# Kernel optimization log

Hardware: AMD Instinct MI355X
Metric: run time of the kernel (lower is better)

## Reference

```python
import jax, jax.numpy as jnp
import numpy as np

DIM = 1024
NUM_HEAD = 16
DIM_HEAD = DIM // NUM_HEAD
MAX_SEQ_LEN = 4096
RMS_EPS = 1.1920928955078125e-07  # torch nn.RMSNorm default eps = finfo(fp32).eps
LIN_EPS = 1e-6
PAD_VAL = 1.0
THETA = 10000.0


def rmsnorm(x, g):
    return x * jax.lax.rsqrt(jnp.mean(x * x, axis=-1, keepdims=True) + RMS_EPS) * g


def setup_inputs() -> dict:
    key = jax.random.key(0)
    ks = jax.random.split(key, 20)
    B, L, C, D = 4, 2048, 256, DIM
    s = 1.0 / np.sqrt(D)
    inp = {
        "x": jax.random.normal(ks[0], (B, L, D), jnp.float32),
        "context": jax.random.normal(ks[1], (B, C, D), jnp.float32),
        "attn_mask": jax.random.randint(ks[2], (B, L, L), 0, 2).astype(bool),
        "start_pos": jax.random.randint(ks[3], (B,), 0, MAX_SEQ_LEN - L).astype(jnp.int64),
        "Wqkv": jax.random.normal(ks[4], (D, 3 * D), jnp.float32) * s,
        "bqkv": jax.random.normal(ks[5], (3 * D,), jnp.float32) * 0.01,
        "g_q": jnp.ones((D,), jnp.float32),
        "g_k": jnp.ones((D,), jnp.float32),
        "cWqkv": jax.random.normal(ks[6], (D, 3 * D), jnp.float32) * s,
        "cbqkv": jax.random.normal(ks[7], (3 * D,), jnp.float32) * 0.01,
        "cg_q": jnp.ones((D,), jnp.float32),
        "cg_k": jnp.ones((D,), jnp.float32),
        "Wout": jax.random.normal(ks[8], (D, D), jnp.float32) * s,
        "bout": jax.random.normal(ks[9], (D,), jnp.float32) * 0.01,
        "g_out": jnp.ones((D,), jnp.float32),
        "cWout": jax.random.normal(ks[10], (D, D), jnp.float32) * s,
        "cbout": jax.random.normal(ks[11], (D,), jnp.float32) * 0.01,
        "cg_out": jnp.ones((D,), jnp.float32),
    }
    return inp


def _freqs(pos_indices):
    # pos_indices: (B, L) int
    inv = 1.0 / (THETA ** (jnp.arange(0, DIM_HEAD, 2, dtype=jnp.float32) / DIM_HEAD))  # (DH/2,)
    ang = pos_indices.astype(jnp.float32)[..., None] * inv  # (B, L, DH/2)
    return jnp.cos(ang), jnp.sin(ang)


def _apply_rope(t, cos, sin):
    # t: (B, H, L, DH); cos/sin: (B, L, DH/2) -> broadcast over head
    B, H, L, DH = t.shape
    tr = t.reshape(B, H, L, DH // 2, 2)
    t0, t1 = tr[..., 0], tr[..., 1]
    c = cos[:, None]  # (B,1,L,DH/2)
    s = sin[:, None]
    out = jnp.stack([t0 * c - t1 * s, t0 * s + t1 * c], axis=-1)
    return out.reshape(B, H, L, DH)


def _split_heads(t):
    B, L, D = t.shape
    return t.reshape(B, L, NUM_HEAD, DIM_HEAD).transpose(0, 2, 1, 3)


def _augment_mask(m, C):
    # m: (B, L, L) bool -> (B, L+C, L+C) bool
    B, L, _ = m.shape
    c_to_seq = jnp.broadcast_to(jnp.any(m, axis=1, keepdims=True), (B, C, L))
    seq_to_c = jnp.broadcast_to(jnp.any(m, axis=2, keepdims=True), (B, L, C))
    c_to_c = jnp.ones((B, C, C), bool)
    top = jnp.concatenate([m, seq_to_c], axis=2)
    bot = jnp.concatenate([c_to_seq, c_to_c], axis=2)
    return jnp.concatenate([top, bot], axis=1)


def reference(x, context, attn_mask, start_pos, Wqkv, bqkv, g_q, g_k,
              cWqkv, cbqkv, cg_q, cg_k, Wout, bout, g_out, cWout, cbout, cg_out):
    B, L, D = x.shape
    C = context.shape[1]

    q, k, v = jnp.split(x @ Wqkv + bqkv, 3, axis=-1)
    q = rmsnorm(q, g_q)
    k = rmsnorm(k, g_k)
    q, k, v = _split_heads(q), _split_heads(k), _split_heads(v)  # (B,H,L,DH)

    pos = start_pos[:, None] + jnp.arange(L, dtype=start_pos.dtype)[None]  # (B,L)
    cos, sin = _freqs(pos)
    q = _apply_rope(q, cos, sin)
    k = _apply_rope(k, cos, sin)

    cq, ck, cv = jnp.split(context @ cWqkv + cbqkv, 3, axis=-1)
    cq = rmsnorm(cq, cg_q)
    ck = rmsnorm(ck, cg_k)
    cq, ck, cv = _split_heads(cq), _split_heads(ck), _split_heads(cv)

    q = jnp.concatenate([q, cq], axis=2)  # (B,H,S,DH), S=L+C
    k = jnp.concatenate([k, ck], axis=2)
    v = jnp.concatenate([v, cv], axis=2)

    full_mask = _augment_mask(attn_mask, C)[:, None]  # (B,1,S,S)

    # linear attention: ReLU feature map + padded-value trick
    qf = jax.nn.relu(q)
    kf = jax.nn.relu(k)
    k_mask = full_mask[:, :, 0, :][..., None].astype(kf.dtype)  # (B,1,S,1)
    kf = kf * k_mask
    vpad = jnp.pad(v, ((0, 0), (0, 0), (0, 0), (0, 1)), constant_values=PAD_VAL)  # (B,H,S,DH+1)
    vk = jnp.einsum('bhse,bhsd->bhed', vpad, kf)        # (B,H,DH+1,DH)
    res = jnp.einsum('bhed,bhqd->bhqe', vk, qf)          # (B,H,S,DH+1)
    attn = res[..., :-1] / (res[..., -1:] + LIN_EPS)     # (B,H,S,DH)

    attn = attn.transpose(0, 2, 1, 3).reshape(B, L + C, D)
    x_out = rmsnorm(attn[:, :L] @ Wout + bout, g_out)
    c_out = rmsnorm(attn[:, L:] @ cWout + cbout, cg_out)
    return x_out, c_out
```

## Files before the change

### kernel.cpp

```cpp
#include <hip/hip_runtime.h>

typedef __bf16 bf16;
typedef __bf16 bf16x4 __attribute__((ext_vector_type(4)));
typedef __bf16 bf16x8 __attribute__((ext_vector_type(8)));
typedef float  floatx4 __attribute__((ext_vector_type(4)));

#define L_SEQ   2048
#define C_SEQ   256
#define S_SEQ   2304
#define NBATCH  4
#define NHEAD   16
#define DHEAD   64
#define DMODEL  1024
#define RMS_EPS 1.1920928955078125e-07f
#define LIN_EPS 1e-6f

__device__ __forceinline__ void gload_lds16(const void* g, void* l) {
  __builtin_amdgcn_global_load_lds(
      (const __attribute__((address_space(1))) void*)g,
      (__attribute__((address_space(3))) void*)l, 16, 0, 0);
}

__device__ __forceinline__ void transpose_job64(
    const float* __restrict__ src, bf16* __restrict__ dst,
    int R, int C, int tb, bf16 (*tile)[65]) {
  int tilesx = C >> 6;
  int c0 = (tb % tilesx) * 64, r0 = (tb / tilesx) * 64;
  int tx = threadIdx.x & 15, ty = threadIdx.x >> 4;
#pragma unroll
  for (int it = 0; it < 4; it++) {
    int rl = ty + it * 16;
    floatx4 v = *(const floatx4*)(src + (size_t)(r0 + rl) * C + c0 + tx * 4);
#pragma unroll
    for (int j = 0; j < 4; j++) tile[tx * 4 + j][rl] = (bf16)v[j];
  }
  __syncthreads();
#pragma unroll
  for (int it = 0; it < 4; it++) {
    int i = ty + it * 16;
    bf16x4 o = *(const bf16x4*)&tile[i][tx * 4];
    *(bf16x4*)(dst + (size_t)(c0 + i) * R + r0 + tx * 4) = o;
  }
}

__device__ __forceinline__ void convert_job(
    const float* __restrict__ src, bf16* __restrict__ dst, int tb) {
  size_t i = ((size_t)tb * 256 + threadIdx.x) * 8;
  floatx4 a = *(const floatx4*)(src + i);
  floatx4 b = *(const floatx4*)(src + i + 4);
  bf16x8 o;
#pragma unroll
  for (int j = 0; j < 4; j++) { o[j] = (bf16)a[j]; o[4 + j] = (bf16)b[j]; }
  *(bf16x8*)(dst + i) = o;
}

__global__ __launch_bounds__(256) void prep(
    const float* __restrict__ Wqkv, const float* __restrict__ cWqkv,
    const float* __restrict__ x, const float* __restrict__ ctx,
    const int* __restrict__ mask, const int* __restrict__ spos,
    bf16* __restrict__ WqkvT, bf16* __restrict__ cWqkvT,
    bf16* __restrict__ xbf, bf16* __restrict__ cbf,
    float* __restrict__ rope, int* __restrict__ anym) {
  __shared__ bf16 tile[64][65];
  __shared__ int sh;
  int b = blockIdx.x;
  if (b < 768) { transpose_job64(Wqkv, WqkvT, 1024, 3072, b, tile); return; }
  b -= 768;
  if (b < 768) { transpose_job64(cWqkv, cWqkvT, 1024, 3072, b, tile); return; }
  b -= 768;
  if (b < 4096) { convert_job(x, xbf, b); return; }
  b -= 4096;
  if (b < 512) { convert_job(ctx, cbf, b); return; }
  b -= 512;
  if (b < 2048) {
    int t = threadIdx.x;
    int tok = b * 4 + (t >> 6);
    int bb = tok >> 11, s = tok & 2047;
    int j = t & 63, fi = j >> 1;
    float ang = (float)(spos[bb] + s) * expf((float)fi * -0.28782313662425572f);
    rope[(size_t)tok * 64 + j] = (j & 1) ? sinf(ang) : cosf(ang);
    return;
  }
  b -= 2048;
  int a = 0;
  size_t base = (size_t)b * L_SEQ * L_SEQ;
  for (int j = threadIdx.x; j < L_SEQ; j += 256) a |= mask[base + j];
  if (threadIdx.x == 0) sh = 0;
  __syncthreads();
  if (a) atomicOr(&sh, 1);
  __syncthreads();
  if (threadIdx.x == 0) anym[b] = sh;
}

__global__ __launch_bounds__(512, 2) void gemm_qkv8(
    const bf16* __restrict__ A1, const bf16* __restrict__ A2,
    const bf16* __restrict__ B1t, const bf16* __restrict__ B2t,
    const float* __restrict__ bias1, const float* __restrict__ bias2,
    bf16* __restrict__ qs, bf16* __restrict__ ks, bf16* __restrict__ vs,
    int K, int ybound, int rpb1, int soff1, int rpb2, int soff2) {
  __shared__ bf16 As[2][256 * 64];
  __shared__ bf16 Bs[2][256 * 64];

  int nwg = gridDim.x * gridDim.y;
  int wg = blockIdx.y * gridDim.x + blockIdx.x;
  int cpx = nwg >> 3;
  wg = (wg & 7) * cpx + (wg >> 3);
  int bx = wg % gridDim.x, by = wg / gridDim.x;
  int n0 = bx * 256;
  const bf16 *Ap, *Bt;
  const float* bias;
  int m0, rpb, soff;
  if (by < ybound) {
    Ap = A1; Bt = B1t; bias = bias1; m0 = by * 256; rpb = rpb1; soff = soff1;
  } else {
    Ap = A2; Bt = B2t; bias = bias2; m0 = (by - ybound) * 256; rpb = rpb2; soff = soff2;
  }

  int t = threadIdx.x, lane = t & 63, w = t >> 6;
  int wr = w >> 2, wc = w & 3;
  int l16 = lane & 15, l4 = lane >> 4;

  int lr = lane >> 3;
  int lcol = ((lane & 7) ^ lr) << 3;
  const bf16* Ag = Ap + (size_t)(m0 + lr) * K + lcol;
  const bf16* Bg = Bt + (size_t)(n0 + lr) * K + lcol;

  int cB0 = w * 2;
  int cB1 = 16 + w * 2;
  int cAX = ((w & 4) << 2) + (w & 3) * 2;
  int cAY = 8 + cAX;

  auto stg = [&](const bf16* G, bf16* Ldst, int c0, int kb) {
#pragma unroll
    for (int j = 0; j < 2; j++) {
      int c = c0 + j;
      gload_lds16(G + (size_t)(c * 8) * K + kb, (char*)Ldst + c * 1024);
    }
  };
  auto ldf = [&](const bf16* S, int row, int ks) {
    return *(const bf16x8*)&S[row * 64 + ((((ks << 2) + l4) ^ (l16 & 7)) << 3)];
  };

  floatx4 acc[8][4] = {};
  int NT = K >> 6;
  stg(Bg, Bs[0], cB0, 0);  stg(Bg, Bs[0], cB1, 0);
  stg(Ag, As[0], cAX, 0);  stg(Ag, As[0], cAY, 0);
  if (NT > 1) {
    stg(Bg, Bs[1], cB0, 64); stg(Bg, Bs[1], cB1, 64);
    stg(Ag, As[1], cAX, 64);
  }
  asm volatile("s_waitcnt vmcnt(6)" ::: "memory");
  __builtin_amdgcn_s_barrier();

  int pb = 0;
  bf16x8 bfr[4][2];
  for (int tt = 0; tt < NT; ++tt) {
    int kb = tt << 6;
    const bf16* Asp = As[pb];
    const bf16* Bsp = Bs[pb];
#pragma unroll
    for (int p = 0; p < 4; ++p) {
      if (p == 0) {
#pragma unroll
        for (int nt = 0; nt < 4; nt++) {
          bfr[nt][0] = ldf(Bsp, wc * 64 + nt * 16 + l16, 0);
          bfr[nt][1] = ldf(Bsp, wc * 64 + nt * 16 + l16, 1);
        }
      }
      int ar = wr * 128 + p * 32 + l16;
      bf16x8 a00 = ldf(Asp, ar, 0);
      bf16x8 a01 = ldf(Asp, ar, 1);
      bf16x8 a10 = ldf(Asp, ar + 16, 0);
      bf16x8 a11 = ldf(Asp, ar + 16, 1);
      if (p == 0)      { if (tt + 1 < NT) stg(Ag, As[pb ^ 1], cAY, kb + 64); }
      else if (p == 1) { if (tt + 2 < NT) stg(Bg, Bs[pb], cB0, kb + 128); }
      else if (p == 2) { if (tt + 2 < NT) stg(Bg, Bs[pb], cB1, kb + 128); }
      else             { if (tt + 2 < NT) stg(Ag, As[pb], cAX, kb + 128); }
      __builtin_amdgcn_s_barrier();
      __builtin_amdgcn_s_setprio(1);
      int mt = p * 2;
#pragma unroll
      for (int nt = 0; nt < 4; nt++) {
        acc[mt][nt]     = __builtin_amdgcn_mfma_f32_16x16x32_bf16(a00, bfr[nt][0], acc[mt][nt], 0, 0, 0);
        acc[mt][nt]     = __builtin_amdgcn_mfma_f32_16x16x32_bf16(a01, bfr[nt][1], acc[mt][nt], 0, 0, 0);
        acc[mt + 1][nt] = __builtin_amdgcn_mfma_f32_16x16x32_bf16(a10, bfr[nt][0], acc[mt + 1][nt], 0, 0, 0);
        acc[mt + 1][nt] = __builtin_amdgcn_mfma_f32_16x16x32_bf16(a11, bfr[nt][1], acc[mt + 1][nt], 0, 0, 0);
      }
      __builtin_amdgcn_s_setprio(0);
      if (p == 3) {
        if (tt + 2 < NT) asm volatile("s_waitcnt vmcnt(6)" ::: "memory");
        else             asm volatile("s_waitcnt vmcnt(0)" ::: "memory");
      }
      __builtin_amdgcn_s_barrier();
    }
    pb ^= 1;
  }

#pragma unroll
  for (int mt = 0; mt < 8; mt++)
#pragma unroll
    for (int nt = 0; nt < 4; nt++) {
      int col = n0 + wc * 64 + nt * 16 + l16;
      float bval = bias[col];
      int which = col >> 10;
      int h = (col >> 6) & 15;
      int dh = col & 63;
      int rmask = (1 << rpb) - 1;
      if (which == 2) {
        int rw0 = m0 + wr * 128 + mt * 16 + l4 * 4;
        int b = rw0 >> rpb;
        int s = soff + (rw0 & rmask);
        bf16x4 o;
#pragma unroll
        for (int r = 0; r < 4; r++) o[r] = (bf16)(acc[mt][nt][r] + bval);
        *(bf16x4*)(vs + ((size_t)(b * NHEAD + h) * DHEAD + dh) * S_SEQ + s) = o;
      } else {
        bf16* dst = which == 0 ? qs : ks;
#pragma unroll
        for (int r = 0; r < 4; r++) {
          int rw = m0 + wr * 128 + mt * 16 + l4 * 4 + r;
          int b = rw >> rpb;
          int s = soff + (rw & rmask);
          dst[((size_t)(b * NHEAD + h) * S_SEQ + s) * DHEAD + dh] =
              (bf16)(acc[mt][nt][r] + bval);
        }
      }
    }
}

template <bool SCATTER>
__global__ __launch_bounds__(256) void gemm_bias(
    const bf16* __restrict__ A1, const bf16* __restrict__ A2,
    const bf16* __restrict__ B1t, const bf16* __restrict__ B2t,
    const float* __restrict__ bias1, const float* __restrict__ bias2,
    bf16* __restrict__ C1, bf16* __restrict__ C2,
    bf16* __restrict__ qs, bf16* __restrict__ ks, bf16* __restrict__ vs,
    int N, int K, int ybound,
    int rpb1, int soff1, int rpb2, int soff2) {
  __shared__ bf16 As[2][4096];
  __shared__ bf16 Bs[2][4096];
  int nwg = gridDim.x * gridDim.y;
  int wg = blockIdx.y * gridDim.x + blockIdx.x;
  int cpx = nwg >> 3;
  wg = (wg & 7) * cpx + (wg >> 3);
  int bx = wg % gridDim.x, by = wg / gridDim.x;
  int n0 = bx * 128;
  const bf16 *Ap, *Bt;
  const float* bias;
  bf16* Cp;
  int m0, rpb, soff;
  if (by < ybound) {
    Ap = A1; Bt = B1t; bias = bias1; Cp = C1;
    m0 = by * 128; rpb = rpb1; soff = soff1;
  } else {
    Ap = A2; Bt = B2t; bias = bias2; Cp = C2;
    m0 = (by - ybound) * 128; rpb = rpb2; soff = soff2;
  }
  int t = threadIdx.x, lane = t & 63, w = t >> 6;
  int wm = (w & 1) * 64, wn = (w >> 1) * 64;
  int l16 = lane & 15, l4 = lane >> 4;
  int crow = w * 32 + (lane >> 2);
  int scol = ((((lane & 3) - ((lane >> 3) & 3)) & 3)) << 3;
  const bf16* Ab = Ap + (size_t)(m0 + crow) * K + scol;
  const bf16* Bb = Bt + (size_t)(n0 + crow) * K + scol;
  auto stage = [&](int buf, int kb) {
#pragma unroll
    for (int j = 0; j < 2; j++) {
      gload_lds16(Ab + (size_t)(j * 16) * K + kb, (char*)As[buf] + (w * 2 + j) * 1024);
      gload_lds16(Bb + (size_t)(j * 16) * K + kb, (char*)Bs[buf] + (w * 2 + j) * 1024);
    }
  };
  int co = ((l4 + ((l16 >> 1) & 3)) & 3) << 3;
  int rba = (wm + l16) * 32 + co;
  int rbb = (wn + l16) * 32 + co;
  floatx4 acc[4][4] = {};
  stage(0, 0);
  __syncthreads();
  int NTt = K >> 5;
  for (int tt = 0; tt < NTt; ++tt) {
    int p = tt & 1;
    if (tt + 1 < NTt) stage(p ^ 1, (tt + 1) << 5);
    bf16x8 bfr[4];
#pragma unroll
    for (int nt = 0; nt < 4; nt++) bfr[nt] = *(const bf16x8*)&Bs[p][rbb + nt * 512];
    __builtin_amdgcn_s_setprio(1);
#pragma unroll
    for (int mt = 0; mt < 4; mt++) {
      bf16x8 a = *(const bf16x8*)&As[p][rba + mt * 512];
#pragma unroll
      for (int nt = 0; nt < 4; nt++)
        acc[mt][nt] = __builtin_amdgcn_mfma_f32_16x16x32_bf16(a, bfr[nt], acc[mt][nt], 0, 0, 0);
    }
    __builtin_amdgcn_s_setprio(0);
    __syncthreads();
  }
#pragma unroll
  for (int mt = 0; mt < 4; mt++)
#pragma unroll
    for (int nt = 0; nt < 4; nt++) {
      int col = n0 + wn + nt * 16 + l16;
      float bval = bias[col];
      if constexpr (SCATTER) {
        int which = col >> 10;
        int h = (col >> 6) & 15;
        int dh = col & 63;
        int rmask = (1 << rpb) - 1;
        if (which == 2) {
          int rw0 = m0 + wm + mt * 16 + l4 * 4;
          int b = rw0 >> rpb;
          int s = soff + (rw0 & rmask);
          bf16x4 o;
#pragma unroll
          for (int r = 0; r < 4; r++) o[r] = (bf16)(acc[mt][nt][r] + bval);
          *(bf16x4*)(vs + ((size_t)(b * NHEAD + h) * DHEAD + dh) * S_SEQ + s) = o;
        } else {
          bf16* dst = which == 0 ? qs : ks;
#pragma unroll
          for (int r = 0; r < 4; r++) {
            int rw = m0 + wm + mt * 16 + l4 * 4 + r;
            int b = rw >> rpb;
            int s = soff + (rw & rmask);
            dst[((size_t)(b * NHEAD + h) * S_SEQ + s) * DHEAD + dh] =
                (bf16)(acc[mt][nt][r] + bval);
          }
        }
      } else {
#pragma unroll
        for (int r = 0; r < 4; r++) {
          int rw = m0 + wm + mt * 16 + l4 * 4 + r;
          Cp[(size_t)rw * N + col] = (bf16)(acc[mt][nt][r] + bval);
        }
      }
    }
}

__global__ __launch_bounds__(256) void qkv_post(
    bf16* __restrict__ qs, bf16* __restrict__ ks,
    const int* __restrict__ mask, const float* __restrict__ rope,
    const int* __restrict__ anym,
    const float* __restrict__ g_q, const float* __restrict__ g_k,
    const float* __restrict__ cg_q, const float* __restrict__ cg_k,
    const float* __restrict__ Wout, const float* __restrict__ cWout,
    bf16* __restrict__ WoutT, bf16* __restrict__ cWoutT,
    float* __restrict__ vkw) {
  __shared__ bf16 tile[64][65];
  __shared__ float red[8];
  int blk = blockIdx.x, t = threadIdx.x;
  if (blk >= 4608) {
    int b = blk - 4608;
    if (b < 256) { transpose_job64(Wout, WoutT, 1024, 1024, b, tile); return; }
    b -= 256;
    if (b < 256) { transpose_job64(cWout, cWoutT, 1024, 1024, b, tile); return; }
    b -= 256;
    int i = b * 1024 + t * 4;
    *(floatx4*)(vkw + i) = floatx4{0.f, 0.f, 0.f, 0.f};
    return;
  }
  int tt = t & 127, tsel = t >> 7;
  int g = blk * 2 + tsel;
  bool is_ctx = g >= NBATCH * L_SEQ;
  int b, s;
  const float *gq, *gk;
  float mval;
  if (!is_ctx) {
    b = g >> 11;
    int l = g & 2047;
    s = l;
    mval = mask[(size_t)b * L_SEQ * L_SEQ + l] ? 1.f : 0.f;
    gq = g_q; gk = g_k;
  } else {
    int gg = g - NBATCH * L_SEQ;
    b = gg >> 8;
    s = L_SEQ + (gg & 255);
    mval = anym[b] ? 1.f : 0.f;
    gq = cg_q; gk = cg_k;
  }
  int d0 = tt * 8;
  int h = tt >> 3, dh = (tt & 7) * 8;
  size_t base = ((size_t)(b * NHEAD + h) * S_SEQ + s) * DHEAD + dh;
  bf16x8 q8 = *(const bf16x8*)(qs + base);
  bf16x8 k8 = *(const bf16x8*)(ks + base);
  float qv[8], kv[8], pq = 0.f, pk = 0.f;
#pragma unroll
  for (int i = 0; i < 8; i++) {
    qv[i] = (float)q8[i]; kv[i] = (float)k8[i];
    pq += qv[i] * qv[i];  pk += kv[i] * kv[i];
  }
  int w = t >> 6;
  for (int off = 32; off > 0; off >>= 1) {
    pq += __shfl_down(pq, off, 64);
    pk += __shfl_down(pk, off, 64);
  }
  if ((t & 63) == 0) { red[w] = pq; red[4 + w] = pk; }
  __syncthreads();
  float sq = red[tsel * 2] + red[tsel * 2 + 1];
  float sk = red[4 + tsel * 2] + red[4 + tsel * 2 + 1];
  float scq = rsqrtf(sq * (1.f / DMODEL) + RMS_EPS);
  float sck = rsqrtf(sk * (1.f / DMODEL) + RMS_EPS);
#pragma unroll
  for (int i = 0; i < 8; i++) {
    qv[i] *= scq * gq[d0 + i];
    kv[i] *= sck * gk[d0 + i];
  }
  if (!is_ctx) {
    floatx4 ta = *(const floatx4*)&rope[((size_t)g) * 64 + dh];
    floatx4 tb = *(const floatx4*)&rope[((size_t)g) * 64 + dh + 4];
#pragma unroll
    for (int pr = 0; pr < 4; pr++) {
      float cc = pr < 2 ? ta[2 * pr] : tb[2 * (pr - 2)];
      float ss = pr < 2 ? ta[2 * pr + 1] : tb[2 * (pr - 2) + 1];
      float t0 = qv[2 * pr], t1 = qv[2 * pr + 1];
      qv[2 * pr]     = t0 * cc - t1 * ss;
      qv[2 * pr + 1] = t0 * ss + t1 * cc;
      t0 = kv[2 * pr]; t1 = kv[2 * pr + 1];
      kv[2 * pr]     = t0 * cc - t1 * ss;
      kv[2 * pr + 1] = t0 * ss + t1 * cc;
    }
  }
  bf16x8 qo, ko;
#pragma unroll
  for (int i = 0; i < 8; i++) {
    qo[i] = (bf16)fmaxf(qv[i], 0.f);
    ko[i] = (bf16)(fmaxf(kv[i], 0.f) * mval);
  }
  *(bf16x8*)(qs + base) = qo;
  *(bf16x8*)(ks + base) = ko;
}

#define VK_CH   12
#define VK_SPAN (S_SEQ / VK_CH)
__global__ __launch_bounds__(256) void vk_mfma(
    const bf16* __restrict__ vT, const bf16* __restrict__ kf,
    float* __restrict__ vk) {
  __shared__ bf16 Vs[2][64][40];
  __shared__ bf16 Ks[2][64][40];
  int bh = blockIdx.x / VK_CH, chunk = blockIdx.x % VK_CH;
  int t = threadIdx.x, lane = t & 63, w = t >> 6;
  int l16 = lane & 15, l4 = lane >> 4;
  const bf16* vp = vT + (size_t)bh * DHEAD * S_SEQ;
  const bf16* kp = kf + (size_t)bh * S_SEQ * DHEAD;
  int s_begin = chunk * VK_SPAN;
  int ve = t >> 2, vso = (t & 3) * 8;
  int ks_s = t & 31, kd0 = (t >> 5) * 8;
  floatx4 acc[4] = {};
  float dsum[8] = {};
  bf16x8 vv = *(const bf16x8*)(vp + (size_t)ve * S_SEQ + s_begin + vso);
  bf16x8 kv = *(const bf16x8*)(kp + (size_t)(s_begin + ks_s) * DHEAD + kd0);
  for (int st = 0; st < VK_SPAN; st += 32) {
    int cur = (st >> 5) & 1;
    *(bf16x8*)&Vs[cur][ve][vso] = vv;
#pragma unroll
    for (int j = 0; j < 8; j++) {
      Ks[cur][kd0 + j][ks_s] = kv[j];
      dsum[j] += (float)kv[j];
    }
    if (st + 32 < VK_SPAN) {
      int s0 = s_begin + st + 32;
      vv = *(const bf16x8*)(vp + (size_t)ve * S_SEQ + s0 + vso);
      kv = *(const bf16x8*)(kp + (size_t)(s0 + ks_s) * DHEAD + kd0);
    }
    __syncthreads();
    bf16x8 af = *(const bf16x8*)&Vs[cur][w * 16 + l16][l4 * 8];
#pragma unroll
    for (int nt = 0; nt < 4; nt++) {
      bf16x8 bfr = *(const bf16x8*)&Ks[cur][nt * 16 + l16][l4 * 8];
      acc[nt] = __builtin_amdgcn_mfma_f32_16x16x32_bf16(af, bfr, acc[nt], 0, 0, 0);
    }
  }
  float* vkbh = vk + (size_t)bh * 65 * 64;
#pragma unroll
  for (int nt = 0; nt < 4; nt++)
#pragma unroll
    for (int r = 0; r < 4; r++)
      atomicAdd(&vkbh[(w * 16 + l4 * 4 + r) * 64 + nt * 16 + l16], acc[nt][r]);
#pragma unroll
  for (int j = 0; j < 8; j++)
#pragma unroll
    for (int off = 16; off > 0; off >>= 1)
      dsum[j] += __shfl_down(dsum[j], off, 32);
  if ((lane & 31) == 0)
#pragma unroll
    for (int j = 0; j < 8; j++)
      atomicAdd(&vkbh[64 * 64 + kd0 + j], dsum[j]);
}

__global__ __launch_bounds__(256) void res_attn(
    const bf16* __restrict__ qf, const float* __restrict__ vk,
    bf16* __restrict__ attn_x, bf16* __restrict__ attn_c) {
  __shared__ bf16 Bs[80][72];
  __shared__ float sden[256];
  int bh = blockIdx.x / 9, mblk = blockIdx.x % 9;
  int b = bh >> 4, h = bh & 15;
  int t = threadIdx.x, lane = t & 63, w = t >> 6;
  const float* vkp = vk + (size_t)bh * 65 * 64;
  for (int i = t; i < 80 * 64; i += 256) {
    int e = i >> 6, d = i & 63;
    Bs[e][d] = (bf16)(e < 65 ? vkp[i] : 0.f);
  }
  __syncthreads();
  int l16 = lane & 15, l4 = lane >> 4;
  const bf16* qbase = qf + (size_t)bh * S_SEQ * DHEAD;
  int q0w = mblk * 256 + w * 64;

  floatx4 acc[4][5] = {};
  bf16x8 af[4][2], bfr[5][2];
#pragma unroll
  for (int mt = 0; mt < 4; mt++) {
    int q = q0w + mt * 16 + l16;
    af[mt][0] = *(const bf16x8*)(qbase + (size_t)q * 64 + l4 * 8);
    af[mt][1] = *(const bf16x8*)(qbase + (size_t)q * 64 + 32 + l4 * 8);
  }
#pragma unroll
  for (int nt = 0; nt < 5; nt++) {
    bfr[nt][0] = *(const bf16x8*)&Bs[nt * 16 + l16][l4 * 8];
    bfr[nt][1] = *(const bf16x8*)&Bs[nt * 16 + l16][32 + l4 * 8];
  }
#pragma unroll
  for (int mt = 0; mt < 4; mt++)
#pragma unroll
    for (int nt = 0; nt < 5; nt++) {
      acc[mt][nt] = __builtin_amdgcn_mfma_f32_16x16x32_bf16(af[mt][0], bfr[nt][0], acc[mt][nt], 0, 0, 0);
      acc[mt][nt] = __builtin_amdgcn_mfma_f32_16x16x32_bf16(af[mt][1], bfr[nt][1], acc[mt][nt], 0, 0, 0);
    }
  if (l16 == 0) {
#pragma unroll
    for (int mt = 0; mt < 4; mt++)
#pragma unroll
      for (int r = 0; r < 4; r++)
        sden[w * 64 + mt * 16 + l4 * 4 + r] = acc[mt][4][r];
  }
  __syncthreads();
#pragma unroll
  for (int mt = 0; mt < 4; mt++)
#pragma unroll
    for (int r = 0; r < 4; r++) {
      float den = sden[w * 64 + mt * 16 + l4 * 4 + r] + LIN_EPS;
      float rden = 1.f / den;
      int q = q0w + mt * 16 + l4 * 4 + r;
#pragma unroll
      for (int nt = 0; nt < 4; nt++) {
        int dcol = nt * 16 + l16;
        float a = acc[mt][nt][r] * rden;
        if (q < L_SEQ)
          attn_x[((size_t)b * L_SEQ + q) * DMODEL + h * DHEAD + dcol] = (bf16)a;
        else
          attn_c[((size_t)b * C_SEQ + (q - L_SEQ)) * DMODEL + h * DHEAD + dcol] = (bf16)a;
      }
    }
}

__global__ __launch_bounds__(256) void final_norm(
    const bf16* __restrict__ y_x, const bf16* __restrict__ y_c,
    const float* __restrict__ g_out, const float* __restrict__ cg_out,
    float* __restrict__ out) {
  __shared__ float red[8];
  int t = threadIdx.x;
  int tt = t & 127, tsel = t >> 7;
  int g = blockIdx.x * 2 + tsel;
  const bf16* src;
  const float* gv;
  if (g < NBATCH * L_SEQ) {
    src = y_x + (size_t)g * DMODEL; gv = g_out;
  } else {
    int gg = g - NBATCH * L_SEQ;
    src = y_c + (size_t)gg * DMODEL; gv = cg_out;
  }
  float* dst = out + (size_t)g * DMODEL;
  int d0 = tt * 8;
  bf16x8 y8 = *(const bf16x8*)(src + d0);
  float yv[8], p = 0.f;
#pragma unroll
  for (int i = 0; i < 8; i++) { yv[i] = (float)y8[i]; p += yv[i] * yv[i]; }
  int w = t >> 6;
  for (int off = 32; off > 0; off >>= 1) p += __shfl_down(p, off, 64);
  if ((t & 63) == 0) red[w] = p;
  __syncthreads();
  float ssum = red[tsel * 2] + red[tsel * 2 + 1];
  float sc = rsqrtf(ssum * (1.f / DMODEL) + RMS_EPS);
  floatx4 o0, o1;
#pragma unroll
  for (int i = 0; i < 4; i++) {
    o0[i] = yv[i] * sc * gv[d0 + i];
    o1[i] = yv[4 + i] * sc * gv[d0 + 4 + i];
  }
  *(floatx4*)(dst + d0) = o0;
  *(floatx4*)(dst + d0 + 4) = o1;
}

extern "C" void kernel_launch(void* const* d_in, const int* in_sizes, int n_in,
                              void* d_out, int out_size, void* d_ws, size_t ws_size,
                              hipStream_t stream) {
  const float* x      = (const float*)d_in[0];
  const float* ctx    = (const float*)d_in[1];
  const int*   mask   = (const int*)d_in[2];
  const int*   spos   = (const int*)d_in[3];
  const float* Wqkv   = (const float*)d_in[4];
  const float* bqkv   = (const float*)d_in[5];
  const float* g_q    = (const float*)d_in[6];
  const float* g_k    = (const float*)d_in[7];
  const float* cWqkv  = (const float*)d_in[8];
  const float* cbqkv  = (const float*)d_in[9];
  const float* cg_q   = (const float*)d_in[10];
  const float* cg_k   = (const float*)d_in[11];
  const float* Wout   = (const float*)d_in[12];
  const float* bout   = (const float*)d_in[13];
  const float* g_out  = (const float*)d_in[14];
  const float* cWout  = (const float*)d_in[15];
  const float* cbout  = (const float*)d_in[16];
  const float* cg_out = (const float*)d_in[17];

  char* wsp = (char*)d_ws;
  size_t off = 0;
  auto alloc = [&](size_t bytes) -> void* {
    void* p = wsp + off;
    off += (bytes + 255) & ~(size_t)255;
    return p;
  };
  bf16* WqkvT  = (bf16*)alloc((size_t)3072 * 1024 * 2);
  bf16* cWqkvT = (bf16*)alloc((size_t)3072 * 1024 * 2);
  bf16* WoutT  = (bf16*)alloc((size_t)1024 * 1024 * 2);
  bf16* cWoutT = (bf16*)alloc((size_t)1024 * 1024 * 2);
  bf16* xbf    = (bf16*)alloc((size_t)NBATCH * L_SEQ * DMODEL * 2);
  bf16* cbf    = (bf16*)alloc((size_t)NBATCH * C_SEQ * DMODEL * 2);
  const size_t SLAB = (size_t)NBATCH * NHEAD * S_SEQ * DHEAD;
  bf16* qfs    = (bf16*)alloc(SLAB * 2);
  bf16* kfs    = (bf16*)alloc(SLAB * 2);
  bf16* vfs    = (bf16*)alloc(SLAB * 2);
  float* vkw   = (float*)alloc((size_t)64 * 65 * 64 * 4);
  float* rope  = (float*)alloc((size_t)NBATCH * L_SEQ * 64 * 4);
  int* anym    = (int*)alloc(256);
  bf16* attn_x = kfs;
  bf16* attn_c = kfs + (size_t)NBATCH * L_SEQ * DMODEL;
  bf16* y_x    = vfs;
  bf16* y_c    = vfs + (size_t)NBATCH * L_SEQ * DMODEL;

  prep<<<8196, 256, 0, stream>>>(Wqkv, cWqkv, x, ctx, mask, spos,
                                 WqkvT, cWqkvT, xbf, cbf, rope, anym);

  gemm_qkv8<<<dim3(12, 36), 512, 0, stream>>>(
      xbf, cbf, WqkvT, cWqkvT, bqkv, cbqkv,
      qfs, kfs, vfs, 1024, 32, 11, 0, 8, L_SEQ);

  qkv_post<<<5380, 256, 0, stream>>>(
      qfs, kfs, mask, rope, anym, g_q, g_k, cg_q, cg_k,
      Wout, cWout, WoutT, cWoutT, vkw);

  vk_mfma<<<64 * VK_CH, 256, 0, stream>>>(vfs, kfs, vkw);

  res_attn<<<576, 256, 0, stream>>>(qfs, vkw, attn_x, attn_c);

  gemm_bias<false><<<dim3(8, 72), 256, 0, stream>>>(
      attn_x, attn_c, WoutT, cWoutT, bout, cbout, y_x, y_c,
      nullptr, nullptr, nullptr, 1024, 1024, 64, 0, 0, 0, 0);

  final_norm<<<4608, 256, 0, stream>>>(
      y_x, y_c, g_out, cg_out, (float*)d_out);
}
```

Before: 345.7 us.

## Restructure QKV GEMM to BK=32 tiles with a simpler double-buffered pipeline

Rewrites the QKV projection GEMM main loop to use 32-wide K tiles instead of 64, halving LDS per buffer and replacing the four-phase interleaved staging with one stage per iteration. All A/B fragments are loaded up front, then 32 MFMAs are issued, with the next-next tile prefetched via direct global-to-LDS loads. The launch bound no longer requests two blocks per CU, and a new swizzle pattern is used for the 32-column layout. It trades fewer barriers per MFMA and smaller LDS for more loop iterations and less fine-grained overlap.

```diff
diff --git a/kernel.cpp b/kernel.cpp
--- a/kernel.cpp
+++ b/kernel.cpp
@@ -92,14 +92,14 @@
   if (threadIdx.x == 0) anym[b] = sh;
 }
 
-__global__ __launch_bounds__(512, 2) void gemm_qkv8(
+__global__ __launch_bounds__(512) void gemm_qkv_bk32(
     const bf16* __restrict__ A1, const bf16* __restrict__ A2,
     const bf16* __restrict__ B1t, const bf16* __restrict__ B2t,
     const float* __restrict__ bias1, const float* __restrict__ bias2,
     bf16* __restrict__ qs, bf16* __restrict__ ks, bf16* __restrict__ vs,
     int K, int ybound, int rpb1, int soff1, int rpb2, int soff2) {
-  __shared__ bf16 As[2][256 * 64];
-  __shared__ bf16 Bs[2][256 * 64];
+  __shared__ bf16 As[2][256 * 32];
+  __shared__ bf16 Bs[2][256 * 32];
 
   int nwg = gridDim.x * gridDim.y;
   int wg = blockIdx.y * gridDim.x + blockIdx.x;
@@ -120,80 +120,51 @@
   int wr = w >> 2, wc = w & 3;
   int l16 = lane & 15, l4 = lane >> 4;
 
-  int lr = lane >> 3;
-  int lcol = ((lane & 7) ^ lr) << 3;
-  const bf16* Ag = Ap + (size_t)(m0 + lr) * K + lcol;
-  const bf16* Bg = Bt + (size_t)(n0 + lr) * K + lcol;
-
-  int cB0 = w * 2;
-  int cB1 = 16 + w * 2;
-  int cAX = ((w & 4) << 2) + (w & 3) * 2;
-  int cAY = 8 + cAX;
-
-  auto stg = [&](const bf16* G, bf16* Ldst, int c0, int kb) {
+  int crow = w * 32 + (lane >> 2);
+  int scol = ((((lane & 3) - ((lane >> 3) & 3)) & 3)) << 3;
+  const bf16* Ab = Ap + (size_t)(m0 + crow) * K + scol;
+  const bf16* Bb = Bt + (size_t)(n0 + crow) * K + scol;
+
+  auto stage = [&](int buf, int kb) {
 #pragma unroll
     for (int j = 0; j < 2; j++) {
-      int c = c0 + j;
-      gload_lds16(G + (size_t)(c * 8) * K + kb, (char*)Ldst + c * 1024);
+      gload_lds16(Ab + (size_t)(j * 16) * K + kb, (char*)As[buf] + (w * 2 + j) * 1024);
+      gload_lds16(Bb + (size_t)(j * 16) * K + kb, (char*)Bs[buf] + (w * 2 + j) * 1024);
     }
   };
-  auto ldf = [&](const bf16* S, int row, int ks) {
-    return *(const bf16x8*)&S[row * 64 + ((((ks << 2) + l4) ^ (l16 & 7)) << 3)];
-  };
+
+  int co = ((l4 + ((l16 >> 1) & 3)) & 3) << 3;
+  int rba = (wr * 128 + l16) * 32 + co;
+  int rbb = (wc * 64 + l16) * 32 + co;
 
   floatx4 acc[8][4] = {};
-  int NT = K >> 6;
-  stg(Bg, Bs[0], cB0, 0);  stg(Bg, Bs[0], cB1, 0);
-  stg(Ag, As[0], cAX, 0);  stg(Ag, As[0], cAY, 0);
-  if (NT > 1) {
-    stg(Bg, Bs[1], cB0, 64); stg(Bg, Bs[1], cB1, 64);
-    stg(Ag, As[1], cAX, 64);
-  }
-  asm volatile("s_waitcnt vmcnt(6)" ::: "memory");
+  int NT = K >> 5;
+  stage(0, 0);
+  stage(1, 32);
+  asm volatile("s_waitcnt vmcnt(4)" ::: "memory");
   __builtin_amdgcn_s_barrier();
 
-  int pb = 0;
-  bf16x8 bfr[4][2];
   for (int tt = 0; tt < NT; ++tt) {
-    int kb = tt << 6;
-    const bf16* Asp = As[pb];
-    const bf16* Bsp = Bs[pb];
-#pragma unroll
-    for (int p = 0; p < 4; ++p) {
-      if (p == 0) {
-#pragma unroll
-        for (int nt = 0; nt < 4; nt++) {
-          bfr[nt][0] = ldf(Bsp, wc * 64 + nt * 16 + l16, 0);
-          bfr[nt][1] = ldf(Bsp, wc * 64 + nt * 16 + l16, 1);
-        }
-      }
-      int ar = wr * 128 + p * 32 + l16;
-      bf16x8 a00 = ldf(Asp, ar, 0);
-      bf16x8 a01 = ldf(Asp, ar, 1);
-      bf16x8 a10 = ldf(Asp, ar + 16, 0);
-      bf16x8 a11 = ldf(Asp, ar + 16, 1);
-      if (p == 0)      { if (tt + 1 < NT) stg(Ag, As[pb ^ 1], cAY, kb + 64); }
-      else if (p == 1) { if (tt + 2 < NT) stg(Bg, Bs[pb], cB0, kb + 128); }
-      else if (p == 2) { if (tt + 2 < NT) stg(Bg, Bs[pb], cB1, kb + 128); }
-      else             { if (tt + 2 < NT) stg(Ag, As[pb], cAX, kb + 128); }
-      __builtin_amdgcn_s_barrier();
-      __builtin_amdgcn_s_setprio(1);
-      int mt = p * 2;
-#pragma unroll
-      for (int nt = 0; nt < 4; nt++) {
-        acc[mt][nt]     = __builtin_amdgcn_mfma_f32_16x16x32_bf16(a00, bfr[nt][0], acc[mt][nt], 0, 0, 0);
-        acc[mt][nt]     = __builtin_amdgcn_mfma_f32_16x16x32_bf16(a01, bfr[nt][1], acc[mt][nt], 0, 0, 0);
-        acc[mt + 1][nt] = __builtin_amdgcn_mfma_f32_16x16x32_bf16(a10, bfr[nt][0], acc[mt + 1][nt], 0, 0, 0);
-        acc[mt + 1][nt] = __builtin_amdgcn_mfma_f32_16x16x32_bf16(a11, bfr[nt][1], acc[mt + 1][nt], 0, 0, 0);
-      }
-      __builtin_amdgcn_s_setprio(0);
-      if (p == 3) {
-        if (tt + 2 < NT) asm volatile("s_waitcnt vmcnt(6)" ::: "memory");
-        else             asm volatile("s_waitcnt vmcnt(0)" ::: "memory");
-      }
-      __builtin_amdgcn_s_barrier();
-    }
-    pb ^= 1;
+    int p = tt & 1;
+    bf16x8 bfr[4], afr[8];
+#pragma unroll
+    for (int nt = 0; nt < 4; nt++) bfr[nt] = *(const bf16x8*)&Bs[p][rbb + nt * 512];
+#pragma unroll
+    for (int mt = 0; mt < 8; mt++) afr[mt] = *(const bf16x8*)&As[p][rba + mt * 512];
+    asm volatile("s_waitcnt lgkmcnt(0)" ::: "memory");
+    __builtin_amdgcn_sched_barrier(0);
+    __builtin_amdgcn_s_barrier();
+    if (tt + 2 < NT) stage(p, (tt + 2) << 5);
+    __builtin_amdgcn_s_setprio(1);
+#pragma unroll
+    for (int mt = 0; mt < 8; mt++)
+#pragma unroll
+      for (int nt = 0; nt < 4; nt++)
+        acc[mt][nt] = __builtin_amdgcn_mfma_f32_16x16x32_bf16(afr[mt], bfr[nt], acc[mt][nt], 0, 0, 0);
+    __builtin_amdgcn_s_setprio(0);
+    if (tt + 2 < NT) asm volatile("s_waitcnt vmcnt(4)" ::: "memory");
+    else             asm volatile("s_waitcnt vmcnt(0)" ::: "memory");
+    __builtin_amdgcn_s_barrier();
   }
 
 #pragma unroll
@@ -637,7 +608,7 @@
   prep<<<8196, 256, 0, stream>>>(Wqkv, cWqkv, x, ctx, mask, spos,
                                  WqkvT, cWqkvT, xbf, cbf, rope, anym);
 
-  gemm_qkv8<<<dim3(12, 36), 512, 0, stream>>>(
+  gemm_qkv_bk32<<<dim3(12, 36), 512, 0, stream>>>(
       xbf, cbf, WqkvT, cWqkvT, bqkv, cbqkv,
       qfs, kfs, vfs, 1024, 32, 11, 0, 8, L_SEQ);
 
```

After: 350.4 us. Within noise of the previous version (+1.3%).
